# Kernel optimization log

Measured on AMD Instinct MI355X. Metric: run time of the kernel, lower is better.

Reference implementation:

```python
import jax, jax.numpy as jnp
import numpy as np

EMB = 1024
HEADS = 16
BLOCK = 128


def setup_inputs() -> dict:
    key = jax.random.key(0)
    k1, k2, k3 = jax.random.split(key, 3)
    B, T, C = 4, 4096, EMB
    x = jax.random.normal(k1, (B, T, C), dtype=jnp.float32)
    # Linear weights stored as [in, out] (i.e. torch W.T); qkv has no bias.
    W_qkv = jax.random.normal(k2, (C, 3 * C), dtype=jnp.float32) * 0.02
    W_proj = jax.random.normal(k3, (C, C), dtype=jnp.float32) * 0.02
    b_proj = jnp.zeros((C,), dtype=jnp.float32)
    return {"x": x, "W_qkv": W_qkv, "W_proj": W_proj, "b_proj": b_proj}


def reference(x, W_qkv, W_proj, b_proj):
    # Dropout is inference-mode identity.
    B, T, C = x.shape
    H, D, BS = HEADS, C // HEADS, BLOCK
    nb = T // BS  # number of local blocks
    qkv = x @ W_qkv  # [B,T,3C]
    q, k, v = jnp.split(qkv, 3, axis=-1)
    # [B, nb, BS, H, D] -- each block attends only within itself
    q = q.reshape(B, nb, BS, H, D)
    k = k.reshape(B, nb, BS, H, D)
    v = v.reshape(B, nb, BS, H, D)
    scores = jnp.einsum("bnqhd,bnkhd->bnhqk", q, k) / jnp.sqrt(jnp.float32(D))
    # is_decoder: causal tril within each diagonal block (tril[i:end, i:end])
    tril = jnp.tril(jnp.ones((BS, BS), dtype=bool))
    scores = jnp.where(tril, scores, -jnp.inf)
    # faithful to original: stable exp, then divide by (sum + 1e-6)
    scores = scores - jnp.max(scores, axis=-1, keepdims=True)
    e = jnp.exp(scores)
    p = e / (jnp.sum(e, axis=-1, keepdims=True) + 1e-6)
    out = jnp.einsum("bnhqk,bnkhd->bnqhd", p, v).reshape(B, T, C)
    return out @ W_proj + b_proj
```

## Files before the change

### kernel.cpp

```cpp
#include <hip/hip_runtime.h>
#include <hip/hip_bf16.h>
#include <math.h>


typedef __bf16 bf16_t;
typedef __bf16 bf16x8 __attribute__((ext_vector_type(8)));
typedef float  f32x4  __attribute__((ext_vector_type(4)));

typedef const __attribute__((address_space(1))) void* gptr_t;
typedef __attribute__((address_space(3))) void* lptr_t;

__global__ __launch_bounds__(256) void cvt_f32_bf16(const float* __restrict__ in,
                                                    bf16_t* __restrict__ out, size_t n) {
    size_t stride = (size_t)gridDim.x * blockDim.x * 4;
    for (size_t i = ((size_t)blockIdx.x * blockDim.x + threadIdx.x) * 4; i < n; i += stride) {
        float4 v = *(const float4*)(in + i);
        bf16_t t[4];
        t[0] = (bf16_t)v.x; t[1] = (bf16_t)v.y; t[2] = (bf16_t)v.z; t[3] = (bf16_t)v.w;
        *(uint2*)(out + i) = *(uint2*)t;
    }
}

__global__ __launch_bounds__(256) void transpose_cvt(const float* __restrict__ in,
                                                     bf16_t* __restrict__ out, int K, int N) {
    __shared__ float tile[32][33];
    const int tx = threadIdx.x & 31, ty = threadIdx.x >> 5;
    const int bx = blockIdx.x, by = blockIdx.y;
    #pragma unroll
    for (int i = 0; i < 4; i++) {
        const int k = by * 32 + ty + i * 8;
        tile[ty + i * 8][tx] = in[(size_t)k * N + bx * 32 + tx];
    }
    __syncthreads();
    #pragma unroll
    for (int i = 0; i < 4; i++) {
        const int n = bx * 32 + ty + i * 8;
        out[(size_t)n * K + by * 32 + tx] = (bf16_t)tile[tx][ty + i * 8];
    }
}

template <bool BF16_OUT, bool BIAS>
__global__ __launch_bounds__(256) void gemm_bt(const bf16_t* __restrict__ A,
                                               const bf16_t* __restrict__ Bt,
                                               void* __restrict__ Cout,
                                               const float* __restrict__ bias,
                                               int M, int N, int K) {
    __shared__ bf16_t As[2][128 * 32];
    __shared__ bf16_t Bs[2][128 * 32];

    const int bn = blockIdx.x, bm = blockIdx.y;
    const int tid = threadIdx.x;
    const int lane = tid & 63, wave = tid >> 6;
    const int wm = wave >> 1, wn = wave & 1;
    const int quad = lane >> 4, l16 = lane & 15;

    const bf16_t* Ab = A  + (size_t)bm * 128 * K;
    const bf16_t* Bb = Bt + (size_t)bn * 128 * K;

    f32x4 acc[4][4];
    for (int i = 0; i < 4; i++)
        for (int j = 0; j < 4; j++)
            acc[i][j] = (f32x4){0.f, 0.f, 0.f, 0.f};

    const int srow = lane >> 2;
    const int scb  = (lane & 3) * 16;

    for (int k0 = 0; k0 < K; k0 += 64) {
        #pragma unroll
        for (int half = 0; half < 2; half++) {
            #pragma unroll
            for (int i = 0; i < 2; i++) {
                const int s = wave * 2 + i;
                const int row = s * 16 + srow;
                const int kk = k0 + half * 32;
                __builtin_amdgcn_global_load_lds(
                    (gptr_t)((const char*)(Ab + (size_t)row * K + kk) + scb),
                    (lptr_t)&As[half][s * 512], 16, 0, 0);
                __builtin_amdgcn_global_load_lds(
                    (gptr_t)((const char*)(Bb + (size_t)row * K + kk) + scb),
                    (lptr_t)&Bs[half][s * 512], 16, 0, 0);
            }
        }
        __syncthreads();

        #pragma unroll
        for (int half = 0; half < 2; half++) {
            bf16x8 af[4], bf[4];
            #pragma unroll
            for (int mr = 0; mr < 4; mr++)
                af[mr] = *(const bf16x8*)&As[half][(wm * 64 + mr * 16 + l16) * 32 + quad * 8];
            #pragma unroll
            for (int nr = 0; nr < 4; nr++)
                bf[nr] = *(const bf16x8*)&Bs[half][(wn * 64 + nr * 16 + l16) * 32 + quad * 8];
            #pragma unroll
            for (int mr = 0; mr < 4; mr++)
                #pragma unroll
                for (int nr = 0; nr < 4; nr++)
                    acc[mr][nr] = __builtin_amdgcn_mfma_f32_16x16x32_bf16(af[mr], bf[nr], acc[mr][nr], 0, 0, 0);
        }
        __syncthreads();
    }

    #pragma unroll
    for (int mr = 0; mr < 4; mr++) {
        #pragma unroll
        for (int nr = 0; nr < 4; nr++) {
            const int gcol = bn * 128 + wn * 64 + nr * 16 + l16;
            #pragma unroll
            for (int reg = 0; reg < 4; reg++) {
                const int grow = bm * 128 + wm * 64 + mr * 16 + quad * 4 + reg;
                float v = acc[mr][nr][reg];
                if (BIAS) v += bias[gcol];
                if (BF16_OUT)
                    ((bf16_t*)Cout)[(size_t)grow * N + gcol] = (bf16_t)v;
                else
                    ((float*)Cout)[(size_t)grow * N + gcol] = v;
            }
        }
    }
}

__global__ __launch_bounds__(256, 3) void attn_kernel(const bf16_t* __restrict__ qkv,
                                                      bf16_t* __restrict__ attn_out) {
    __shared__ __align__(16) char smem[54272];
    bf16_t* qs = (bf16_t*)smem;
    bf16_t* ks = (bf16_t*)(smem + 18432);
    bf16_t* vT = (bf16_t*)(smem + 36864);
    bf16_t* ps = (bf16_t*)smem;

    const int tid = threadIdx.x;
    const int lane = tid & 63, wave = tid >> 6;
    const int quad = lane >> 4, l16 = lane & 15;

    const int bid = blockIdx.x;
    const int h = bid & 15;
    const int blk = (bid >> 4) & 31;
    const int b = bid >> 9;
    const int row0 = (b * 32 + blk) * 128;
    const int LDQ = 3072;

    for (int t = tid; t < 128 * 8; t += 256) {
        const int r = t >> 3;
        const int c = (t & 7) * 8;
        const bf16_t* src = qkv + (size_t)(row0 + r) * LDQ + h * 64;
        *(uint4*)&qs[r * 72 + c] = *(const uint4*)(src + c);
        *(uint4*)&ks[r * 72 + c] = *(const uint4*)(src + 1024 + c);
        bf16x8 vv = *(const bf16x8*)(src + 2048 + c);
        #pragma unroll
        for (int j = 0; j < 8; j++)
            vT[(c + j) * 136 + r] = vv[j];
    }
    __syncthreads();

    f32x4 sfrag[2][8];
    for (int mr = 0; mr < 2; mr++)
        for (int nc = 0; nc < 8; nc++)
            sfrag[mr][nc] = (f32x4){0.f, 0.f, 0.f, 0.f};

    #pragma unroll
    for (int ksl = 0; ksl < 2; ksl++) {
        bf16x8 aq[2], bk[8];
        #pragma unroll
        for (int mr = 0; mr < 2; mr++)
            aq[mr] = *(const bf16x8*)&qs[(wave * 32 + mr * 16 + l16) * 72 + ksl * 32 + quad * 8];
        #pragma unroll
        for (int nc = 0; nc < 8; nc++)
            bk[nc] = *(const bf16x8*)&ks[(nc * 16 + l16) * 72 + ksl * 32 + quad * 8];
        #pragma unroll
        for (int mr = 0; mr < 2; mr++)
            #pragma unroll
            for (int nc = 0; nc < 8; nc++)
                sfrag[mr][nc] = __builtin_amdgcn_mfma_f32_16x16x32_bf16(aq[mr], bk[nc], sfrag[mr][nc], 0, 0, 0);
    }

    #pragma unroll
    for (int mr = 0; mr < 2; mr++) {
        #pragma unroll
        for (int nc = 0; nc < 8; nc++) {
            #pragma unroll
            for (int reg = 0; reg < 4; reg++) {
                const int row = wave * 32 + mr * 16 + quad * 4 + reg;
                const int col = nc * 16 + l16;
                float s = sfrag[mr][nc][reg] * 0.125f;
                if (col > row) s = -INFINITY;
                sfrag[mr][nc][reg] = s;
            }
        }
    }

    #pragma unroll
    for (int mr = 0; mr < 2; mr++) {
        #pragma unroll
        for (int reg = 0; reg < 4; reg++) {
            float m = -INFINITY;
            #pragma unroll
            for (int nc = 0; nc < 8; nc++) m = fmaxf(m, sfrag[mr][nc][reg]);
            #pragma unroll
            for (int off = 1; off < 16; off <<= 1) m = fmaxf(m, __shfl_xor(m, off));
            float sum = 0.f;
            #pragma unroll
            for (int nc = 0; nc < 8; nc++) {
                float e = __expf(sfrag[mr][nc][reg] - m);
                sfrag[mr][nc][reg] = e;
                sum += e;
            }
            #pragma unroll
            for (int off = 1; off < 16; off <<= 1) sum += __shfl_xor(sum, off);
            const float inv = 1.0f / (sum + 1e-6f);
            #pragma unroll
            for (int nc = 0; nc < 8; nc++) sfrag[mr][nc][reg] *= inv;
        }
    }

    __syncthreads();

    #pragma unroll
    for (int mr = 0; mr < 2; mr++)
        #pragma unroll
        for (int nc = 0; nc < 8; nc++)
            #pragma unroll
            for (int reg = 0; reg < 4; reg++) {
                const int row = wave * 32 + mr * 16 + quad * 4 + reg;
                const int col = nc * 16 + l16;
                ps[row * 136 + col] = (bf16_t)sfrag[mr][nc][reg];
            }
    __syncthreads();

    f32x4 oacc[2][4];
    for (int mr = 0; mr < 2; mr++)
        for (int nd = 0; nd < 4; nd++)
            oacc[mr][nd] = (f32x4){0.f, 0.f, 0.f, 0.f};

    #pragma unroll
    for (int ksl = 0; ksl < 4; ksl++) {
        bf16x8 ap[2];
        #pragma unroll
        for (int mr = 0; mr < 2; mr++)
            ap[mr] = *(const bf16x8*)&ps[(wave * 32 + mr * 16 + l16) * 136 + ksl * 32 + quad * 8];
        #pragma unroll
        for (int nd = 0; nd < 4; nd++) {
            bf16x8 bv = *(const bf16x8*)&vT[(nd * 16 + l16) * 136 + ksl * 32 + quad * 8];
            #pragma unroll
            for (int mr = 0; mr < 2; mr++)
                oacc[mr][nd] = __builtin_amdgcn_mfma_f32_16x16x32_bf16(ap[mr], bv, oacc[mr][nd], 0, 0, 0);
        }
    }

    #pragma unroll
    for (int mr = 0; mr < 2; mr++)
        #pragma unroll
        for (int nd = 0; nd < 4; nd++)
            #pragma unroll
            for (int reg = 0; reg < 4; reg++) {
                const int row = row0 + wave * 32 + mr * 16 + quad * 4 + reg;
                const int col = h * 64 + nd * 16 + l16;
                attn_out[(size_t)row * 1024 + col] = (bf16_t)oacc[mr][nd][reg];
            }
}

extern "C" void kernel_launch(void* const* d_in, const int* in_sizes, int n_in,
                              void* d_out, int out_size, void* d_ws, size_t ws_size,
                              hipStream_t stream) {
    const float* x     = (const float*)d_in[0];
    const float* Wqkv  = (const float*)d_in[1];
    const float* Wproj = (const float*)d_in[2];
    const float* bproj = (const float*)d_in[3];

    const int M = 16384, C = 1024, N1 = 3072;

    char* ws = (char*)d_ws;
    bf16_t* xb     = (bf16_t*)(ws);
    bf16_t* wqkvT  = (bf16_t*)(ws + 33554432);
    bf16_t* wprojT = (bf16_t*)(ws + 39845888);
    bf16_t* qkvb   = (bf16_t*)(ws + 41943040);
    bf16_t* attnb  = (bf16_t*)(ws + 142606336);

    cvt_f32_bf16<<<8192, 256, 0, stream>>>(x, xb, (size_t)M * C);
    transpose_cvt<<<dim3(N1 / 32, C / 32), 256, 0, stream>>>(Wqkv, wqkvT, C, N1);
    transpose_cvt<<<dim3(C / 32, C / 32), 256, 0, stream>>>(Wproj, wprojT, C, C);

    gemm_bt<true, false><<<dim3(N1 / 128, M / 128), 256, 0, stream>>>(
        xb, wqkvT, (void*)qkvb, nullptr, M, N1, C);

    attn_kernel<<<2048, 256, 0, stream>>>(qkvb, attnb);

    gemm_bt<false, true><<<dim3(C / 128, M / 128), 256, 0, stream>>>(
        attnb, wprojT, d_out, bproj, M, C, C);
}
```

Before: 350.4 us.

## Replace 128x128 GEMM with swizzled, prefetching 256x256-tile GEMM

Both GEMMs (QKV and output projection) now use a 256x256 output tile with 512 threads, 8 waves and a K-step of 64. The shared-memory tiles use an XOR swizzle on 16-byte chunks to cut bank conflicts. The loads for the next K-step are issued into a second buffer while the current step's MFMAs run, and MFMA sections get raised wave priority. This targets redundant global traffic and load/compute serialization, at the cost of 128KB of LDS per block, which limits occupancy to one block per CU.

```diff
diff --git a/kernel.cpp b/kernel.cpp
--- a/kernel.cpp
+++ b/kernel.cpp
@@ -40,75 +40,111 @@
 }
 
 template <bool BF16_OUT, bool BIAS>
-__global__ __launch_bounds__(256) void gemm_bt(const bf16_t* __restrict__ A,
-                                               const bf16_t* __restrict__ Bt,
-                                               void* __restrict__ Cout,
-                                               const float* __restrict__ bias,
-                                               int M, int N, int K) {
-    __shared__ bf16_t As[2][128 * 32];
-    __shared__ bf16_t Bs[2][128 * 32];
-
+__global__ __launch_bounds__(512, 2) void gemm256(const bf16_t* __restrict__ A,
+                                                  const bf16_t* __restrict__ Bt,
+                                                  void* __restrict__ Cout,
+                                                  const float* __restrict__ bias,
+                                                  int M, int N, int K) {
+    __shared__ bf16_t As[2][256 * 64];
+    __shared__ bf16_t Bs[2][256 * 64];
+
+    const int tid  = threadIdx.x;
+    const int lane = tid & 63, wave = tid >> 6;
+    const int quad = lane >> 4, l16 = lane & 15;
+    const int wm = wave >> 2, wn = wave & 3;
     const int bn = blockIdx.x, bm = blockIdx.y;
-    const int tid = threadIdx.x;
-    const int lane = tid & 63, wave = tid >> 6;
-    const int wm = wave >> 1, wn = wave & 1;
-    const int quad = lane >> 4, l16 = lane & 15;
-
-    const bf16_t* Ab = A  + (size_t)bm * 128 * K;
-    const bf16_t* Bb = Bt + (size_t)bn * 128 * K;
-
-    f32x4 acc[4][4];
-    for (int i = 0; i < 4; i++)
-        for (int j = 0; j < 4; j++)
-            acc[i][j] = (f32x4){0.f, 0.f, 0.f, 0.f};
-
-    const int srow = lane >> 2;
-    const int scb  = (lane & 3) * 16;
-
-    for (int k0 = 0; k0 < K; k0 += 64) {
-        #pragma unroll
-        for (int half = 0; half < 2; half++) {
-            #pragma unroll
-            for (int i = 0; i < 2; i++) {
-                const int s = wave * 2 + i;
-                const int row = s * 16 + srow;
-                const int kk = k0 + half * 32;
-                __builtin_amdgcn_global_load_lds(
-                    (gptr_t)((const char*)(Ab + (size_t)row * K + kk) + scb),
-                    (lptr_t)&As[half][s * 512], 16, 0, 0);
-                __builtin_amdgcn_global_load_lds(
-                    (gptr_t)((const char*)(Bb + (size_t)row * K + kk) + scb),
-                    (lptr_t)&Bs[half][s * 512], 16, 0, 0);
-            }
-        }
-        __syncthreads();
-
-        #pragma unroll
-        for (int half = 0; half < 2; half++) {
-            bf16x8 af[4], bf[4];
-            #pragma unroll
-            for (int mr = 0; mr < 4; mr++)
-                af[mr] = *(const bf16x8*)&As[half][(wm * 64 + mr * 16 + l16) * 32 + quad * 8];
-            #pragma unroll
-            for (int nr = 0; nr < 4; nr++)
-                bf[nr] = *(const bf16x8*)&Bs[half][(wn * 64 + nr * 16 + l16) * 32 + quad * 8];
-            #pragma unroll
-            for (int mr = 0; mr < 4; mr++)
+
+    const bf16_t* Ab = A  + (size_t)bm * 256 * K;
+    const bf16_t* Bb = Bt + (size_t)bn * 256 * K;
+
+    const int r0  = tid >> 3;
+    const int c8s = (tid & 7) ^ (r0 & 7);
+    const int swz = l16 & 7;
+
+    f32x4 acc[8][4];
+    #pragma unroll
+    for (int i = 0; i < 8; ++i)
+        #pragma unroll
+        for (int j = 0; j < 4; ++j) acc[i][j] = (f32x4){0.f, 0.f, 0.f, 0.f};
+
+#define STAGE(DST, SRC, H, I, KOFF)                                                   \
+    __builtin_amdgcn_global_load_lds(                                                 \
+        (gptr_t)((SRC) + (size_t)((H) * 128 + (I) * 64 + r0) * K + (KOFF) + c8s * 8), \
+        (lptr_t)&(DST)[(H) * 8192 + (I) * 4096 + wave * 512], 16, 0, 0)
+
+    STAGE(As[0], Ab, 0, 0, 0); STAGE(As[0], Ab, 0, 1, 0);
+    STAGE(As[0], Ab, 1, 0, 0); STAGE(As[0], Ab, 1, 1, 0);
+    STAGE(Bs[0], Bb, 0, 0, 0); STAGE(Bs[0], Bb, 0, 1, 0);
+    STAGE(Bs[0], Bb, 1, 0, 0); STAGE(Bs[0], Bb, 1, 1, 0);
+    __syncthreads();
+
+    const int NT = K >> 6;
+    for (int t = 0; t < NT; ++t) {
+        const int cur = t & 1;
+        const bool pf = (t + 1) < NT;
+        const int kk = (t + 1) << 6;
+        bf16_t* Asn = As[cur ^ 1];
+        bf16_t* Bsn = Bs[cur ^ 1];
+        const bf16_t* Asc = As[cur];
+        const bf16_t* Bsc = Bs[cur];
+
+        #pragma unroll
+        for (int q = 0; q < 4; ++q) {
+            const int mh = q >> 1, nh = q & 1;
+
+            bf16x8 af[4][2], bf[2][2];
+            #pragma unroll
+            for (int mr = 0; mr < 4; ++mr) {
+                const int arow = wm * 128 + (mh * 4 + mr) * 16 + l16;
                 #pragma unroll
-                for (int nr = 0; nr < 4; nr++)
-                    acc[mr][nr] = __builtin_amdgcn_mfma_f32_16x16x32_bf16(af[mr], bf[nr], acc[mr][nr], 0, 0, 0);
-        }
-        __syncthreads();
-    }
-
-    #pragma unroll
-    for (int mr = 0; mr < 4; mr++) {
-        #pragma unroll
-        for (int nr = 0; nr < 4; nr++) {
-            const int gcol = bn * 128 + wn * 64 + nr * 16 + l16;
-            #pragma unroll
-            for (int reg = 0; reg < 4; reg++) {
-                const int grow = bm * 128 + wm * 64 + mr * 16 + quad * 4 + reg;
+                for (int ks = 0; ks < 2; ++ks)
+                    af[mr][ks] = *(const bf16x8*)&Asc[arow * 64 + ((((ks << 2) | quad) ^ swz) << 3)];
+            }
+            #pragma unroll
+            for (int nr = 0; nr < 2; ++nr) {
+                const int brow = wn * 64 + (nh * 2 + nr) * 16 + l16;
+                #pragma unroll
+                for (int ks = 0; ks < 2; ++ks)
+                    bf[nr][ks] = *(const bf16x8*)&Bsc[brow * 64 + ((((ks << 2) | quad) ^ swz) << 3)];
+            }
+
+            if (q == 0 && pf) {
+                STAGE(Asn, Ab, 0, 0, kk); STAGE(Asn, Ab, 0, 1, kk);
+                STAGE(Asn, Ab, 1, 0, kk); STAGE(Asn, Ab, 1, 1, kk);
+            }
+            if (q == 1 && pf) {
+                STAGE(Bsn, Bb, 0, 0, kk); STAGE(Bsn, Bb, 0, 1, kk);
+                STAGE(Bsn, Bb, 1, 0, kk); STAGE(Bsn, Bb, 1, 1, kk);
+            }
+
+            __builtin_amdgcn_s_barrier();
+            __builtin_amdgcn_s_setprio(1);
+            #pragma unroll
+            for (int mr = 0; mr < 4; ++mr)
+                #pragma unroll
+                for (int nr = 0; nr < 2; ++nr)
+                    #pragma unroll
+                    for (int ks = 0; ks < 2; ++ks)
+                        acc[mh * 4 + mr][nh * 2 + nr] = __builtin_amdgcn_mfma_f32_16x16x32_bf16(
+                            af[mr][ks], bf[nr][ks], acc[mh * 4 + mr][nh * 2 + nr], 0, 0, 0);
+            __builtin_amdgcn_s_setprio(0);
+
+            if (q < 3)
+                __builtin_amdgcn_s_barrier();
+            else
+                __syncthreads();
+        }
+    }
+#undef STAGE
+
+    #pragma unroll
+    for (int mr = 0; mr < 8; ++mr) {
+        #pragma unroll
+        for (int nr = 0; nr < 4; ++nr) {
+            const int gcol = bn * 256 + wn * 64 + nr * 16 + l16;
+            #pragma unroll
+            for (int reg = 0; reg < 4; ++reg) {
+                const int grow = bm * 256 + wm * 128 + mr * 16 + quad * 4 + reg;
                 float v = acc[mr][nr][reg];
                 if (BIAS) v += bias[gcol];
                 if (BF16_OUT)
@@ -279,11 +315,11 @@
     transpose_cvt<<<dim3(N1 / 32, C / 32), 256, 0, stream>>>(Wqkv, wqkvT, C, N1);
     transpose_cvt<<<dim3(C / 32, C / 32), 256, 0, stream>>>(Wproj, wprojT, C, C);
 
-    gemm_bt<true, false><<<dim3(N1 / 128, M / 128), 256, 0, stream>>>(
+    gemm256<true, false><<<dim3(N1 / 256, M / 256), 512, 0, stream>>>(
         xb, wqkvT, (void*)qkvb, nullptr, M, N1, C);
 
     attn_kernel<<<2048, 256, 0, stream>>>(qkvb, attnb);
 
-    gemm_bt<false, true><<<dim3(C / 128, M / 128), 256, 0, stream>>>(
+    gemm256<false, true><<<dim3(C / 256, M / 256), 512, 0, stream>>>(
         attnb, wprojT, d_out, bproj, M, C, C);
 }
```

Measured after the change: 324.9 us. -7.3%, faster.
